# Optimization experiments

Measured on AMD Instinct MI355X. Metric: run time of the kernel, lower is better.

Reference implementation:

```python
import jax, jax.numpy as jnp
import numpy as np
import math

N_HEADS = 8
LN_EPS = 1e-5

def _layernorm(x, g, b):
    m = jnp.mean(x, axis=-1, keepdims=True)
    v = jnp.var(x, axis=-1, keepdims=True)
    return (x - m) / jnp.sqrt(v + LN_EPS) * g + b

def _elu_feature(x):
    return jax.nn.elu(x) + 1.0

def _recurrence(Q, K, V, decay, reverse):
    # Q,K,V: (B,H,T,d); decay: (H,)
    B, H, T, d = Q.shape
    lamS = decay[None, :, None, None]
    lamz = decay[None, :, None]
    def step(carry, inp):
        S, z = carry
        q, k, v = inp
        S = lamS * S + k[..., :, None] * v[..., None, :]       # (B,H,d,d)
        z = lamz * z + k                                        # (B,H,d)
        y_raw = jnp.einsum('bhd,bhde->bhe', q, S)
        c_raw = jnp.sum(q * z, axis=-1)
        qk = jnp.sum(q * k, axis=-1, keepdims=True)
        return (S, z), (y_raw - 0.5 * qk * v, c_raw - 0.5 * qk[..., 0])
    S0 = jnp.zeros((B, H, d, d), Q.dtype)
    z0 = jnp.zeros((B, H, d), Q.dtype)
    qs = jnp.moveaxis(Q, 2, 0)
    ks = jnp.moveaxis(K, 2, 0)
    vs = jnp.moveaxis(V, 2, 0)
    _, (Y, C) = jax.lax.scan(step, (S0, z0), (qs, ks, vs), reverse=reverse)
    return jnp.moveaxis(Y, 0, 2), jnp.moveaxis(C, 0, 2)  # (B,H,T,d),(B,H,T)

def setup_inputs() -> dict:
    B, T, D, F = 2, 2048, 512, 2048
    key = jax.random.key(0)
    ks = jax.random.split(key, 8)
    std = 0.02
    return {
        'x': jax.random.normal(ks[0], (B, T, D), jnp.float32),
        'mask': jnp.zeros((B, T), dtype=bool),
        'Wq': jax.random.normal(ks[1], (D, D), jnp.float32) * std,
        'Wk': jax.random.normal(ks[2], (D, D), jnp.float32) * std,
        'Wv': jax.random.normal(ks[3], (D, D), jnp.float32) * std,
        'Wo': jax.random.normal(ks[4], (D, D), jnp.float32) * std,
        'bo': jnp.zeros((D,), jnp.float32),
        'g1': jnp.ones((D,), jnp.float32),
        'b1': jnp.zeros((D,), jnp.float32),
        'g2': jnp.ones((D,), jnp.float32),
        'b2': jnp.zeros((D,), jnp.float32),
        'W1': jax.random.normal(ks[5], (F, D), jnp.float32) * std,
        'bf1': jnp.zeros((F,), jnp.float32),
        'W2': jax.random.normal(ks[6], (D, F), jnp.float32) * std,
        'bf2': jnp.zeros((D,), jnp.float32),
        'decay_logit': jnp.full((N_HEADS,), math.log(9.0), jnp.float32),
    }

def reference(x, mask, Wq, Wk, Wv, Wo, bo, g1, b1, g2, b2, W1, bf1, W2, bf2, decay_logit):
    B, T, D = x.shape
    H = N_HEADS
    hd = D // H
    residual = x
    xn = _layernorm(x, g1, b1)
    def proj(W):
        return jnp.einsum('btd,od->bto', xn, W).reshape(B, T, H, hd).transpose(0, 2, 1, 3)
    Q = _elu_feature(proj(Wq))
    K = _elu_feature(proj(Wk))
    V = proj(Wv)
    pad = (~mask).astype(x.dtype)[:, None, :, None]  # (B,1,T,1)
    K = K * pad
    V = V * pad
    decay = jax.nn.sigmoid(decay_logit)
    Yf, Cf = _recurrence(Q, K, V, decay, reverse=False)
    Yb, Cb = _recurrence(Q, K, V, decay, reverse=True)
    denom = jnp.clip((Cf + Cb)[..., None], 1e-6)
    out = (Yf + Yb) / denom                       # (B,H,T,d)
    out = out.transpose(0, 2, 1, 3).reshape(B, T, D)
    out = jnp.einsum('btd,od->bto', out, Wo) + bo
    x = residual + out
    h = _layernorm(x, g2, b2)
    ffn = jnp.einsum('btd,fd->btf', h, W1) + bf1
    ffn = jax.nn.gelu(ffn, approximate=False)
    ffn = jnp.einsum('btf,df->btd', ffn, W2) + bf2
    return x + ffn
```

## Files before the change

kernel.cpp:

```cpp
#include <hip/hip_runtime.h>
#include <math.h>

#define BB 2
#define TT 2048
#define DD 512
#define FF 2048
#define HH 8
#define BT 4096
#define NC 32
#define CK 64

typedef __bf16 bf16_t;
typedef bf16_t bf16x8 __attribute__((ext_vector_type(8)));
typedef bf16_t bf16x4 __attribute__((ext_vector_type(4)));
typedef float f32x4 __attribute__((ext_vector_type(4)));

typedef const __attribute__((address_space(1))) void* gas_p;
typedef __attribute__((address_space(3))) void* las_p;

__device__ __forceinline__ void async16(const void* g, void* l) {
  __builtin_amdgcn_global_load_lds((gas_p)g, (las_p)l, 16, 0, 0);
}

#define PIPE_SYNC(vm) asm volatile("s_waitcnt lgkmcnt(0) vmcnt(" vm ")\n\ts_barrier" ::: "memory")

__global__ __launch_bounds__(256) void ln_cast_kernel(
    const float* __restrict__ x, const float* __restrict__ g, const float* __restrict__ bb,
    bf16_t* __restrict__ out,
    const float* __restrict__ Wq, const float* __restrict__ Wk,
    const float* __restrict__ Wv, const float* __restrict__ Wo,
    const float* __restrict__ W1, const float* __restrict__ W2,
    bf16_t* __restrict__ wdst) {
  int t = threadIdx.x;
  if (blockIdx.x >= BT) {
    size_t i = ((size_t)(blockIdx.x - BT) * 256 + t) * 8;
    const float* src; size_t off;
    if (i < 262144)       { src = Wq; off = i; }
    else if (i < 524288)  { src = Wk; off = i - 262144; }
    else if (i < 786432)  { src = Wv; off = i - 524288; }
    else if (i < 1048576) { src = Wo; off = i - 786432; }
    else if (i < 2097152) { src = W1; off = i - 1048576; }
    else                  { src = W2; off = i - 2097152; }
    float4 a = *(const float4*)(src + off);
    float4 b = *(const float4*)(src + off + 4);
    bf16x8 o;
    o[0] = (bf16_t)a.x; o[1] = (bf16_t)a.y; o[2] = (bf16_t)a.z; o[3] = (bf16_t)a.w;
    o[4] = (bf16_t)b.x; o[5] = (bf16_t)b.y; o[6] = (bf16_t)b.z; o[7] = (bf16_t)b.w;
    *(bf16x8*)(wdst + i) = o;
    return;
  }
  int row = blockIdx.x;
  const float* xr = x + (size_t)row * DD;
  float v0 = xr[t], v1 = xr[t + 256];
  float s = v0 + v1, sq = v0 * v0 + v1 * v1;
  for (int o = 32; o; o >>= 1) { s += __shfl_down(s, o); sq += __shfl_down(sq, o); }
  __shared__ float red[8];
  __shared__ float mv[2];
  int w = t >> 6;
  if ((t & 63) == 0) { red[w] = s; red[4 + w] = sq; }
  __syncthreads();
  if (t == 0) {
    float S = red[0] + red[1] + red[2] + red[3];
    float Q = red[4] + red[5] + red[6] + red[7];
    float m = S * (1.f / 512.f);
    float var = Q * (1.f / 512.f) - m * m;
    mv[0] = m; mv[1] = rsqrtf(var + 1e-5f);
  }
  __syncthreads();
  float m = mv[0], r = mv[1];
  out[(size_t)row * DD + t]       = (bf16_t)((v0 - m) * r * g[t] + bb[t]);
  out[(size_t)row * DD + t + 256] = (bf16_t)((v1 - m) * r * g[t + 256] + bb[t + 256]);
}

template<int MODE>
__global__ __launch_bounds__(256) void mfma_gemm(
    const bf16_t* __restrict__ A, const bf16_t* __restrict__ B, int K, int NT,
    bf16_t* __restrict__ Qo, bf16_t* __restrict__ Ko, bf16_t* __restrict__ Vo,
    bf16_t* __restrict__ Ob, const float* __restrict__ bias,
    const unsigned char* __restrict__ mask) {
  __shared__ __align__(16) bf16_t smem[3 * 8192];
  int tid = threadIdx.x;
  int bid = blockIdx.x;
  int xcd = bid & 7;
  int tmp = bid >> 3;
  int nt = tmp % NT;
  int mt = (tmp / NT) * 8 + xcd;
  int n0 = nt * 128, m0 = mt * 128;
  int elt = tid * 8;
  int srow = elt >> 5, scol = elt & 31;
  const bf16_t* Ag = A + (size_t)(m0 + srow) * K + scol;
  const bf16_t* Bg = B + (size_t)(n0 + srow) * K + scol;
  size_t hstep = (size_t)64 * K;
  int NS = K >> 5;
#define ISSUE(s) { bf16_t* st = smem + ((s) % 3) * 8192; int k0 = (s) * 32; \
    async16(Ag + k0, st + elt); async16(Ag + k0 + hstep, st + 2048 + elt); \
    async16(Bg + k0, st + 4096 + elt); async16(Bg + k0 + hstep, st + 6144 + elt); }
  ISSUE(0); ISSUE(1);
  f32x4 acc[4][4] = {};
  int w = tid >> 6, l = tid & 63;
  int wm = (w >> 1) * 64, wn = (w & 1) * 64;
  int fr = l & 15, fk = (l >> 4) * 8;
  for (int i = 0; i < NS; i++) {
    if (i < NS - 1) PIPE_SYNC("4");
    else            PIPE_SYNC("0");
    if (i + 2 < NS) ISSUE(i + 2);
    const bf16_t* As = smem + (i % 3) * 8192;
    const bf16_t* Bs = As + 4096;
    bf16x8 af[4], bfr[4];
#pragma unroll
    for (int ii = 0; ii < 4; ii++) af[ii] = *(const bf16x8*)&As[(wm + ii * 16 + fr) * 32 + fk];
#pragma unroll
    for (int j = 0; j < 4; j++) bfr[j] = *(const bf16x8*)&Bs[(wn + j * 16 + fr) * 32 + fk];
#pragma unroll
    for (int ii = 0; ii < 4; ii++)
#pragma unroll
      for (int j = 0; j < 4; j++)
        acc[ii][j] = __builtin_amdgcn_mfma_f32_16x16x32_bf16(af[ii], bfr[j], acc[ii][j], 0, 0, 0);
  }
#undef ISSUE
  __syncthreads();
  const int CST = 136;
  int cn = l & 15, cr = (l >> 4) * 4;
  bf16_t* outp;
  int ldc, ncol0;
  if (MODE == 0) {
    int seg = n0 >> 9;
    outp = seg == 0 ? Qo : (seg == 1 ? Ko : Vo);
    ldc = 512; ncol0 = n0 & 511;
  } else {
    outp = Ob; ldc = 2048; ncol0 = n0;
  }
#pragma unroll
  for (int i = 0; i < 4; i++) {
#pragma unroll
    for (int r = 0; r < 4; r++) {
      int mrow = wm + i * 16 + cr + r;
      float p = 1.f;
      if (MODE == 0) p = mask[m0 + mrow] ? 0.f : 1.f;
#pragma unroll
      for (int j = 0; j < 4; j++) {
        int ncol = wn + j * 16 + cn;
        float v = acc[i][j][r];
        float ov;
        if (MODE == 0) {
          int seg = n0 >> 9;
          float e = v > 0.f ? v + 1.f : expf(v);
          ov = seg == 0 ? e : (seg == 1 ? e * p : v * p);
        } else {
          float t2 = v + bias[ncol0 + ncol];
          ov = 0.5f * t2 * (1.f + erff(t2 * 0.70710678118654752f));
        }
        smem[mrow * CST + ncol] = (bf16_t)ov;
      }
    }
  }
  __syncthreads();
#pragma unroll
  for (int it = 0; it < 8; it++) {
    int vec = tid + it * 256;
    int row = vec >> 4;
    int col = (vec & 15) * 8;
    bf16x8 v8 = *(const bf16x8*)&smem[row * CST + col];
    *(bf16x8*)(outp + (size_t)(m0 + row) * ldc + ncol0 + col) = v8;
  }
}

template<int KPER>
__global__ __launch_bounds__(256) void mfma_gemm_pk(
    const bf16_t* __restrict__ A, const bf16_t* __restrict__ B, int Kst,
    float* __restrict__ P0, float* __restrict__ P1) {
  __shared__ __align__(16) bf16_t smem[4 * 6144];
  int tid = threadIdx.x;
  int bid = blockIdx.x;
  int xcd = bid & 7;
  int tmp = bid >> 3;
  int nt = tmp & 7;
  int mt = (tmp >> 3) * 8 + xcd;
  int n0 = nt * 64, m0 = mt * 128;
  int kb = blockIdx.y * KPER;
  float* P = blockIdx.y ? P1 : P0;
  int elt = tid * 8;
  int arow = elt >> 5, acol = elt & 31;
  const bf16_t* Ag = A + (size_t)(m0 + arow) * Kst + acol;
  const bf16_t* Bg = B + (size_t)(n0 + arow) * Kst + acol;
  size_t hstep = (size_t)64 * Kst;
  const int NS = KPER >> 5;
#define ISSUE(s) { bf16_t* st = smem + ((s) & 3) * 6144; int k0 = kb + (s) * 32; \
    async16(Ag + k0, st + elt); async16(Ag + k0 + hstep, st + 2048 + elt); \
    async16(Bg + k0, st + 4096 + elt); }
  ISSUE(0); ISSUE(1); ISSUE(2);
  f32x4 acc[4][2] = {};
  int w = tid >> 6, l = tid & 63;
  int wm = (w >> 1) * 64, wn = (w & 1) * 32;
  int fr = l & 15, fk = (l >> 4) * 8;
  for (int i = 0; i < NS; i++) {
    int rem = NS - 1 - i;
    if (rem >= 2)      PIPE_SYNC("6");
    else if (rem == 1) PIPE_SYNC("3");
    else               PIPE_SYNC("0");
    if (i + 3 < NS) ISSUE(i + 3);
    const bf16_t* As = smem + (i & 3) * 6144;
    const bf16_t* Bs = As + 4096;
    bf16x8 af[4], bfr[2];
#pragma unroll
    for (int ii = 0; ii < 4; ii++) af[ii] = *(const bf16x8*)&As[(wm + ii * 16 + fr) * 32 + fk];
#pragma unroll
    for (int j = 0; j < 2; j++) bfr[j] = *(const bf16x8*)&Bs[(wn + j * 16 + fr) * 32 + fk];
#pragma unroll
    for (int ii = 0; ii < 4; ii++)
#pragma unroll
      for (int j = 0; j < 2; j++)
        acc[ii][j] = __builtin_amdgcn_mfma_f32_16x16x32_bf16(af[ii], bfr[j], acc[ii][j], 0, 0, 0);
  }
#undef ISSUE
  int cn = l & 15, cr = (l >> 4) * 4;
#pragma unroll
  for (int i = 0; i < 4; i++)
#pragma unroll
    for (int r = 0; r < 4; r++) {
      int m = m0 + wm + i * 16 + cr + r;
#pragma unroll
      for (int j = 0; j < 2; j++) {
        int n = n0 + wn + j * 16 + cn;
        P[(size_t)m * 512 + n] = acc[i][j][r];
      }
    }
}

__global__ __launch_bounds__(256) void reduce2_kernel(
    const float* __restrict__ P0, const float* __restrict__ P1,
    const float* __restrict__ bias, const float* __restrict__ resid,
    float* __restrict__ o) {
  size_t idx = ((size_t)blockIdx.x * 256 + threadIdx.x) * 4;
  int n = (int)(idx & 511);
  float4 a = *(const float4*)(P0 + idx);
  float4 b = *(const float4*)(P1 + idx);
  float4 rr = *(const float4*)(resid + idx);
  float4 bi = *(const float4*)(bias + n);
  *(float4*)(o + idx) = make_float4(a.x + b.x + bi.x + rr.x, a.y + b.y + bi.y + rr.y,
                                    a.z + b.z + bi.z + rr.z, a.w + b.w + bi.w + rr.w);
}

__global__ __launch_bounds__(256) void reduce_ln_kernel(
    const float* __restrict__ P0, const float* __restrict__ P1,
    const float* __restrict__ bias, const float* __restrict__ resid,
    float* __restrict__ x2, const float* __restrict__ g, const float* __restrict__ bb,
    bf16_t* __restrict__ out) {
  int row = blockIdx.x;
  int t = threadIdx.x;
  size_t o0 = (size_t)row * DD + t;
  size_t o1 = o0 + 256;
  float v0 = P0[o0] + P1[o0] + bias[t] + resid[o0];
  float v1 = P0[o1] + P1[o1] + bias[t + 256] + resid[o1];
  x2[o0] = v0; x2[o1] = v1;
  float s = v0 + v1, sq = v0 * v0 + v1 * v1;
  for (int o = 32; o; o >>= 1) { s += __shfl_down(s, o); sq += __shfl_down(sq, o); }
  __shared__ float red[8];
  __shared__ float mv[2];
  int w = t >> 6;
  if ((t & 63) == 0) { red[w] = s; red[4 + w] = sq; }
  __syncthreads();
  if (t == 0) {
    float S = red[0] + red[1] + red[2] + red[3];
    float Q = red[4] + red[5] + red[6] + red[7];
    float m = S * (1.f / 512.f);
    float var = Q * (1.f / 512.f) - m * m;
    mv[0] = m; mv[1] = rsqrtf(var + 1e-5f);
  }
  __syncthreads();
  float m = mv[0], r = mv[1];
  out[o0] = (bf16_t)((v0 - m) * r * g[t] + bb[t]);
  out[o1] = (bf16_t)((v1 - m) * r * g[t + 256] + bb[t + 256]);
}

__global__ __launch_bounds__(256) void chunk_summary_kernel(
    const bf16_t* __restrict__ Kb, const bf16_t* __restrict__ Vb,
    const float* __restrict__ dl, bf16_t* __restrict__ Sst, float* __restrict__ zst) {
  int chunk = blockIdx.x, bh = blockIdx.y;
  int b = bh >> 3, h = bh & 7;
  int t0 = chunk * CK;
  int tid = threadIdx.x;
  __shared__ __align__(16) float Ks[64][64];
  __shared__ __align__(16) float Vs[64][64];
  __shared__ float pw[72];
  float lam = 1.f / (1.f + expf(-dl[h]));
  if (tid <= 64) pw[tid] = powf(lam, (float)tid);
  int lrow = tid >> 2, lq = tid & 3;
  for (int q = 0; q < 2; q++) {
    int c = lq * 16 + q * 8;
    size_t g = ((size_t)(b * TT + t0 + lrow)) * DD + (size_t)h * 64 + c;
    bf16x8 k8 = *(const bf16x8*)(Kb + g);
    bf16x8 v8 = *(const bf16x8*)(Vb + g);
#pragma unroll
    for (int u = 0; u < 8; u++) { Ks[lrow][c + u] = (float)k8[u]; Vs[lrow][c + u] = (float)v8[u]; }
  }
  __syncthreads();
  int e1 = tid & 63;
  int e2b = (tid >> 6) * 16;
  float af_[16], ab_[16];
#pragma unroll
  for (int r = 0; r < 16; r++) { af_[r] = 0.f; ab_[r] = 0.f; }
  float zf = 0.f, zb = 0.f;
  for (int j = 0; j < 64; j++) {
    float kj = Ks[j][e1];
    float kf = pw[63 - j] * kj;
    float kb2 = pw[j] * kj;
    if (tid < 64) { zf += kf; zb += kb2; }
#pragma unroll
    for (int rr = 0; rr < 16; rr += 4) {
      float4 v4 = *(const float4*)&Vs[j][e2b + rr];
      af_[rr]     += kf * v4.x;  ab_[rr]     += kb2 * v4.x;
      af_[rr + 1] += kf * v4.y;  ab_[rr + 1] += kb2 * v4.y;
      af_[rr + 2] += kf * v4.z;  ab_[rr + 2] += kb2 * v4.z;
      af_[rr + 3] += kf * v4.w;  ab_[rr + 3] += kb2 * v4.w;
    }
  }
  size_t bf_ = (((size_t)bh * NC + chunk) * 64 + e1) * 64 + e2b;
  size_t bb_ = ((((size_t)16 + bh) * NC + chunk) * 64 + e1) * 64 + e2b;
  bf16x8 of0, of1, ob0, ob1;
#pragma unroll
  for (int u = 0; u < 8; u++) {
    of0[u] = (bf16_t)af_[u];     of1[u] = (bf16_t)af_[u + 8];
    ob0[u] = (bf16_t)ab_[u];     ob1[u] = (bf16_t)ab_[u + 8];
  }
  *(bf16x8*)(Sst + bf_) = of0;     *(bf16x8*)(Sst + bf_ + 8) = of1;
  *(bf16x8*)(Sst + bb_) = ob0;     *(bf16x8*)(Sst + bb_ + 8) = ob1;
  if (tid < 64) {
    zst[((size_t)bh * NC + chunk) * 64 + tid] = zf;
    zst[(((size_t)16 + bh) * NC + chunk) * 64 + tid] = zb;
  }
}

__global__ __launch_bounds__(1024) void scan_kernel(bf16_t* __restrict__ Sst,
                                                    float* __restrict__ zst,
                                                    const float* __restrict__ dl) {
  int bh = blockIdx.x, dir = blockIdx.y;
  int h = bh & 7;
  int tid = threadIdx.x;
  float lam = 1.f / (1.f + expf(-dl[h]));
  float lamC = powf(lam, 64.f);
  size_t base = ((size_t)dir * 16 + bh) * (size_t)NC * 4096 + (size_t)tid * 4;
  float s0 = 0.f, s1 = 0.f, s2 = 0.f, s3 = 0.f;
  for (int g = 0; g < 4; g++) {
    bf16x4 L[8];
#pragma unroll
    for (int i = 0; i < 8; i++) {
      int s = g * 8 + i;
      int c = dir ? (NC - 1 - s) : s;
      L[i] = *(bf16x4*)(Sst + base + (size_t)c * 4096);
    }
#pragma unroll
    for (int i = 0; i < 8; i++) {
      int s = g * 8 + i;
      int c = dir ? (NC - 1 - s) : s;
      s0 = s0 * lamC + (float)L[i][0];
      s1 = s1 * lamC + (float)L[i][1];
      s2 = s2 * lamC + (float)L[i][2];
      s3 = s3 * lamC + (float)L[i][3];
      bf16x4 o;
      o[0] = (bf16_t)s0; o[1] = (bf16_t)s1; o[2] = (bf16_t)s2; o[3] = (bf16_t)s3;
      *(bf16x4*)(Sst + base + (size_t)c * 4096) = o;
    }
  }
  if (tid < 64) {
    size_t zb = ((size_t)dir * 16 + bh) * (size_t)NC * 64 + tid;
    float z = 0.f;
    for (int g = 0; g < 4; g++) {
      float zL[8];
#pragma unroll
      for (int i = 0; i < 8; i++) {
        int s = g * 8 + i;
        int c = dir ? (NC - 1 - s) : s;
        zL[i] = zst[zb + (size_t)c * 64];
      }
#pragma unroll
      for (int i = 0; i < 8; i++) {
        int s = g * 8 + i;
        int c = dir ? (NC - 1 - s) : s;
        z = z * lamC + zL[i];
        zst[zb + (size_t)c * 64] = z;
      }
    }
  }
}

__global__ __launch_bounds__(256) void chunk_attn_kernel(
    const bf16_t* __restrict__ Qb, const bf16_t* __restrict__ Kb, const bf16_t* __restrict__ Vb,
    const bf16_t* __restrict__ Sst, const float* __restrict__ zst, const float* __restrict__ dl,
    bf16_t* __restrict__ attnb) {
  int chunk = blockIdx.x, bh = blockIdx.y;
  int b = bh >> 3, h = bh & 7;
  int t0 = chunk * CK;
  int tid = threadIdx.x;
  __shared__ __align__(16) float Qt[64][68];
  __shared__ __align__(16) float KtA[64][68];
  __shared__ __align__(16) float Vs[64][64];
  __shared__ __align__(16) bf16_t Spf[64][64];
  __shared__ __align__(16) bf16_t Spb[64][64];
  __shared__ float rowpart[64][16];
  __shared__ float zpf[64], zpb[64];
  __shared__ float den[64];
  __shared__ float pw[72];
  float lam = 1.f / (1.f + expf(-dl[h]));
  if (tid <= 64) pw[tid] = powf(lam, (float)tid);
  int lrow = tid >> 2, lq = tid & 3;
  for (int q = 0; q < 2; q++) {
    int c = lq * 16 + q * 8;
    size_t g = ((size_t)(b * TT + t0 + lrow)) * DD + (size_t)h * 64 + c;
    bf16x8 q8 = *(const bf16x8*)(Qb + g);
    bf16x8 k8 = *(const bf16x8*)(Kb + g);
    bf16x8 v8 = *(const bf16x8*)(Vb + g);
#pragma unroll
    for (int u = 0; u < 8; u++) {
      Qt[c + u][lrow] = (float)q8[u];
      KtA[c + u][lrow] = (float)k8[u];
      Vs[lrow][c + u] = (float)v8[u];
    }
  }
  {
    int c16 = lq * 16;
    if (chunk > 0) {
      const bf16_t* src = Sst + ((size_t)bh * NC + chunk - 1) * 4096 + (size_t)lrow * 64 + c16;
      *(bf16x8*)&Spf[lrow][c16] = *(const bf16x8*)src;
      *(bf16x8*)&Spf[lrow][c16 + 8] = *(const bf16x8*)(src + 8);
      if (tid < 64) zpf[tid] = zst[((size_t)bh * NC + chunk - 1) * 64 + tid];
    } else {
      bf16x8 z8 = {};
      *(bf16x8*)&Spf[lrow][c16] = z8;
      *(bf16x8*)&Spf[lrow][c16 + 8] = z8;
      if (tid < 64) zpf[tid] = 0.f;
    }
    if (chunk < NC - 1) {
      const bf16_t* src = Sst + (((size_t)16 + bh) * NC + chunk + 1) * 4096 + (size_t)lrow * 64 + c16;
      *(bf16x8*)&Spb[lrow][c16] = *(const bf16x8*)src;
      *(bf16x8*)&Spb[lrow][c16 + 8] = *(const bf16x8*)(src + 8);
      if (tid < 64) zpb[tid] = zst[(((size_t)16 + bh) * NC + chunk + 1) * 64 + tid];
    } else {
      bf16x8 z8 = {};
      *(bf16x8*)&Spb[lrow][c16] = z8;
      *(bf16x8*)&Spb[lrow][c16 + 8] = z8;
      if (tid < 64) zpb[tid] = 0.f;
    }
  }
  __syncthreads();
  int tx = tid & 15, ty = tid >> 4;
  int i0 = ty * 4, j0 = tx * 4;
  int e0 = tx * 4;
  float acc[4][4] = {};
  for (int d = 0; d < 64; d++) {
    float4 qf = *(const float4*)&Qt[d][i0];
    float4 kf = *(const float4*)&KtA[d][j0];
    float qa[4] = {qf.x, qf.y, qf.z, qf.w};
    float ka[4] = {kf.x, kf.y, kf.z, kf.w};
#pragma unroll
    for (int r = 0; r < 4; r++)
#pragma unroll
      for (int c = 0; c < 4; c++) acc[r][c] += qa[r] * ka[c];
  }
  __syncthreads();
  float rs[4] = {0.f, 0.f, 0.f, 0.f};
  float colv[4][4];
#pragma unroll
  for (int r = 0; r < 4; r++) {
    int i = i0 + r;
#pragma unroll
    for (int c = 0; c < 4; c++) {
      int j = j0 + c;
      int dd = i > j ? i - j : j - i;
      float v = acc[r][c] * pw[dd];
      rs[r] += v;
      colv[c][r] = v;
    }
  }
#pragma unroll
  for (int c = 0; c < 4; c++)
    *(float4*)&KtA[j0 + c][i0] = make_float4(colv[c][0], colv[c][1], colv[c][2], colv[c][3]);
#pragma unroll
  for (int r = 0; r < 4; r++) rowpart[i0 + r][tx] = rs[r];
  __syncthreads();
  float accY[4][4] = {}, accSf[4][4] = {}, accSb[4][4] = {};
  for (int j = 0; j < 64; j++) {
    float4 af = *(const float4*)&KtA[j][i0];
    float4 vf = *(const float4*)&Vs[j][e0];
    float aa[4] = {af.x, af.y, af.z, af.w};
    float vv[4] = {vf.x, vf.y, vf.z, vf.w};
#pragma unroll
    for (int r = 0; r < 4; r++)
#pragma unroll
      for (int c = 0; c < 4; c++) accY[r][c] += aa[r] * vv[c];
  }
  for (int d = 0; d < 64; d++) {
    float4 qf = *(const float4*)&Qt[d][i0];
    bf16x4 sf4 = *(const bf16x4*)&Spf[d][e0];
    bf16x4 sb4 = *(const bf16x4*)&Spb[d][e0];
    float qq[4] = {qf.x, qf.y, qf.z, qf.w};
    float sf[4] = {(float)sf4[0], (float)sf4[1], (float)sf4[2], (float)sf4[3]};
    float sb[4] = {(float)sb4[0], (float)sb4[1], (float)sb4[2], (float)sb4[3]};
#pragma unroll
    for (int r = 0; r < 4; r++)
#pragma unroll
      for (int c = 0; c < 4; c++) {
        accSf[r][c] += qq[r] * sf[c];
        accSb[r][c] += qq[r] * sb[c];
      }
  }
  if (tid < 64) {
    int i = tid;
    float s = 0.f;
#pragma unroll
    for (int xx = 0; xx < 16; xx++) s += rowpart[i][xx];
    float czf = 0.f, czb = 0.f;
    for (int d = 0; d < 64; d++) { czf += Qt[d][i] * zpf[d]; czb += Qt[d][i] * zpb[d]; }
    den[i] = s + pw[i + 1] * czf + pw[64 - i] * czb;
  }
  __syncthreads();
#pragma unroll
  for (int r = 0; r < 4; r++) {
    int i = i0 + r;
    float lrf = pw[i + 1], lrb = pw[64 - i];
    float inv = 1.f / fmaxf(den[i], 1e-6f);
    bf16x4 o;
#pragma unroll
    for (int c = 0; c < 4; c++)
      o[c] = (bf16_t)((accY[r][c] + lrf * accSf[r][c] + lrb * accSb[r][c]) * inv);
    *(bf16x4*)(attnb + ((size_t)(b * TT + t0 + i)) * DD + (size_t)h * 64 + e0) = o;
  }
}

extern "C" void kernel_launch(void* const* d_in, const int* in_sizes, int n_in,
                              void* d_out, int out_size, void* d_ws, size_t ws_size,
                              hipStream_t stream) {
  const float* x   = (const float*)d_in[0];
  const unsigned char* mask = (const unsigned char*)d_in[1];
  const float* Wq  = (const float*)d_in[2];
  const float* Wk  = (const float*)d_in[3];
  const float* Wv  = (const float*)d_in[4];
  const float* Wo  = (const float*)d_in[5];
  const float* bo  = (const float*)d_in[6];
  const float* g1  = (const float*)d_in[7];
  const float* b1  = (const float*)d_in[8];
  const float* g2  = (const float*)d_in[9];
  const float* b2  = (const float*)d_in[10];
  const float* W1  = (const float*)d_in[11];
  const float* bf1 = (const float*)d_in[12];
  const float* W2  = (const float*)d_in[13];
  const float* bf2 = (const float*)d_in[14];
  const float* dl  = (const float*)d_in[15];
  float* out = (float*)d_out;

  float* ws = (float*)d_ws;
  const size_t U = (size_t)BT * DD;
  float* Qr  = ws;
  float* Kr  = ws + U;
  float* Vr  = ws + 2 * U;
  float* R3  = ws + 3 * U;
  float* R4  = ws + 4 * U;
  float* x2  = ws + 5 * U;
  bf16_t* Sstb = (bf16_t*)(ws + 6 * U);
  float* zst = ws + 8 * U;
  bf16_t* wall = (bf16_t*)(ws + 8 * U + 131072);
  bf16_t* Qb    = (bf16_t*)Qr;
  bf16_t* Kb    = (bf16_t*)Kr;
  bf16_t* Vb    = (bf16_t*)Vr;
  bf16_t* xnb   = (bf16_t*)R3;
  bf16_t* attnb = (bf16_t*)x2;
  bf16_t* h2b   = (bf16_t*)Qr;
  bf16_t* ffn1b = (bf16_t*)Kr;
  bf16_t* Wob = wall + 786432;
  bf16_t* W1b = wall + 1048576;
  bf16_t* W2b = wall + 2097152;
  float* Ps0 = R3;
  float* Ps1 = R4;

  ln_cast_kernel<<<BT + 1536, 256, 0, stream>>>(x, g1, b1, xnb, Wq, Wk, Wv, Wo, W1, W2, wall);
  mfma_gemm<0><<<384, 256, 0, stream>>>(xnb, wall, 512, 12, Qb, Kb, Vb,
                                        nullptr, nullptr, mask);
  chunk_summary_kernel<<<dim3(NC, 16), 256, 0, stream>>>(Kb, Vb, dl, Sstb, zst);
  scan_kernel<<<dim3(16, 2), 1024, 0, stream>>>(Sstb, zst, dl);
  chunk_attn_kernel<<<dim3(NC, 16), 256, 0, stream>>>(Qb, Kb, Vb, Sstb, zst, dl, attnb);
  mfma_gemm_pk<256><<<dim3(256, 2), 256, 0, stream>>>(attnb, Wob, 512, Ps0, Ps1);
  reduce_ln_kernel<<<BT, 256, 0, stream>>>(Ps0, Ps1, bo, x, x2, g2, b2, h2b);
  mfma_gemm<2><<<512, 256, 0, stream>>>(h2b, W1b, 512, 16, nullptr, nullptr, nullptr,
                                        ffn1b, bf1, nullptr);
  mfma_gemm_pk<1024><<<dim3(256, 2), 256, 0, stream>>>(ffn1b, W2b, 2048, Ps0, Ps1);
  reduce2_kernel<<<2048, 256, 0, stream>>>(Ps0, Ps1, bf2, x2, out);
}
```

Before: 216.6 us.

## Use bf16 MFMA for intra-chunk attention and store chunk states transposed

Replaces the fp32 scalar FMA tiles in chunk_attn_kernel with bf16 16x16x32 MFMA for the QK^T, AV and Q·S products, keeping operands in bf16 padded shared arrays. The chunk-state kernel now writes S transposed so the MFMA B-operand can be loaded row-contiguously. The aim is to cut ALU time in the attention chunk kernel. In exchange, the decayed score matrix is rounded to bf16 before the AV product, which lowers precision, and the state and output stores become scalar and strided rather than vectorised.

Measured after the change: 207.8 us. 1.04x faster.

```diff
diff --git a/kernel.cpp b/kernel.cpp
--- a/kernel.cpp
+++ b/kernel.cpp
@@ -315,16 +315,13 @@
       af_[rr + 3] += kf * v4.w;  ab_[rr + 3] += kb2 * v4.w;
     }
   }
-  size_t bf_ = (((size_t)bh * NC + chunk) * 64 + e1) * 64 + e2b;
-  size_t bb_ = ((((size_t)16 + bh) * NC + chunk) * 64 + e1) * 64 + e2b;
-  bf16x8 of0, of1, ob0, ob1;
-#pragma unroll
-  for (int u = 0; u < 8; u++) {
-    of0[u] = (bf16_t)af_[u];     of1[u] = (bf16_t)af_[u + 8];
-    ob0[u] = (bf16_t)ab_[u];     ob1[u] = (bf16_t)ab_[u + 8];
-  }
-  *(bf16x8*)(Sst + bf_) = of0;     *(bf16x8*)(Sst + bf_ + 8) = of1;
-  *(bf16x8*)(Sst + bb_) = ob0;     *(bf16x8*)(Sst + bb_ + 8) = ob1;
+  size_t bfr = ((size_t)bh * NC + chunk) * 4096;
+  size_t bbr = (((size_t)16 + bh) * NC + chunk) * 4096;
+#pragma unroll
+  for (int r = 0; r < 16; r++) {
+    Sst[bfr + (size_t)(e2b + r) * 64 + e1] = (bf16_t)af_[r];
+    Sst[bbr + (size_t)(e2b + r) * 64 + e1] = (bf16_t)ab_[r];
+  }
   if (tid < 64) {
     zst[((size_t)bh * NC + chunk) * 64 + tid] = zf;
     zst[(((size_t)16 + bh) * NC + chunk) * 64 + tid] = zb;
@@ -384,6 +381,7 @@
   }
 }
 
+#define AST 72
 __global__ __launch_bounds__(256) void chunk_attn_kernel(
     const bf16_t* __restrict__ Qb, const bf16_t* __restrict__ Kb, const bf16_t* __restrict__ Vb,
     const bf16_t* __restrict__ Sst, const float* __restrict__ zst, const float* __restrict__ dl,
@@ -392,11 +390,11 @@
   int b = bh >> 3, h = bh & 7;
   int t0 = chunk * CK;
   int tid = threadIdx.x;
-  __shared__ __align__(16) float Qt[64][68];
-  __shared__ __align__(16) float KtA[64][68];
-  __shared__ __align__(16) float Vs[64][64];
-  __shared__ __align__(16) bf16_t Spf[64][64];
-  __shared__ __align__(16) bf16_t Spb[64][64];
+  __shared__ __align__(16) bf16_t Qa[64 * AST];
+  __shared__ __align__(16) bf16_t KA[64 * AST];
+  __shared__ __align__(16) bf16_t Vt[64 * AST];
+  __shared__ __align__(16) bf16_t Sft[64 * AST];
+  __shared__ __align__(16) bf16_t Sbt[64 * AST];
   __shared__ float rowpart[64][16];
   __shared__ float zpf[64], zpb[64];
   __shared__ float den[64];
@@ -410,99 +408,85 @@
     bf16x8 q8 = *(const bf16x8*)(Qb + g);
     bf16x8 k8 = *(const bf16x8*)(Kb + g);
     bf16x8 v8 = *(const bf16x8*)(Vb + g);
-#pragma unroll
-    for (int u = 0; u < 8; u++) {
-      Qt[c + u][lrow] = (float)q8[u];
-      KtA[c + u][lrow] = (float)k8[u];
-      Vs[lrow][c + u] = (float)v8[u];
-    }
+    *(bf16x8*)&Qa[lrow * AST + c] = q8;
+    *(bf16x8*)&KA[lrow * AST + c] = k8;
+#pragma unroll
+    for (int u = 0; u < 8; u++) Vt[(c + u) * AST + lrow] = v8[u];
   }
   {
     int c16 = lq * 16;
     if (chunk > 0) {
       const bf16_t* src = Sst + ((size_t)bh * NC + chunk - 1) * 4096 + (size_t)lrow * 64 + c16;
-      *(bf16x8*)&Spf[lrow][c16] = *(const bf16x8*)src;
-      *(bf16x8*)&Spf[lrow][c16 + 8] = *(const bf16x8*)(src + 8);
+      *(bf16x8*)&Sft[lrow * AST + c16] = *(const bf16x8*)src;
+      *(bf16x8*)&Sft[lrow * AST + c16 + 8] = *(const bf16x8*)(src + 8);
       if (tid < 64) zpf[tid] = zst[((size_t)bh * NC + chunk - 1) * 64 + tid];
     } else {
       bf16x8 z8 = {};
-      *(bf16x8*)&Spf[lrow][c16] = z8;
-      *(bf16x8*)&Spf[lrow][c16 + 8] = z8;
+      *(bf16x8*)&Sft[lrow * AST + c16] = z8;
+      *(bf16x8*)&Sft[lrow * AST + c16 + 8] = z8;
       if (tid < 64) zpf[tid] = 0.f;
     }
     if (chunk < NC - 1) {
       const bf16_t* src = Sst + (((size_t)16 + bh) * NC + chunk + 1) * 4096 + (size_t)lrow * 64 + c16;
-      *(bf16x8*)&Spb[lrow][c16] = *(const bf16x8*)src;
-      *(bf16x8*)&Spb[lrow][c16 + 8] = *(const bf16x8*)(src + 8);
+      *(bf16x8*)&Sbt[lrow * AST + c16] = *(const bf16x8*)src;
+      *(bf16x8*)&Sbt[lrow * AST + c16 + 8] = *(const bf16x8*)(src + 8);
       if (tid < 64) zpb[tid] = zst[(((size_t)16 + bh) * NC + chunk + 1) * 64 + tid];
     } else {
       bf16x8 z8 = {};
-      *(bf16x8*)&Spb[lrow][c16] = z8;
-      *(bf16x8*)&Spb[lrow][c16 + 8] = z8;
+      *(bf16x8*)&Sbt[lrow * AST + c16] = z8;
+      *(bf16x8*)&Sbt[lrow * AST + c16 + 8] = z8;
       if (tid < 64) zpb[tid] = 0.f;
     }
   }
   __syncthreads();
-  int tx = tid & 15, ty = tid >> 4;
-  int i0 = ty * 4, j0 = tx * 4;
-  int e0 = tx * 4;
-  float acc[4][4] = {};
-  for (int d = 0; d < 64; d++) {
-    float4 qf = *(const float4*)&Qt[d][i0];
-    float4 kf = *(const float4*)&KtA[d][j0];
-    float qa[4] = {qf.x, qf.y, qf.z, qf.w};
-    float ka[4] = {kf.x, kf.y, kf.z, kf.w};
-#pragma unroll
-    for (int r = 0; r < 4; r++)
-#pragma unroll
-      for (int c = 0; c < 4; c++) acc[r][c] += qa[r] * ka[c];
+  int w = tid >> 6, l = tid & 63;
+  int fr = l & 15, fk = (l >> 4) * 8;
+  int cr = (l >> 4) * 4, cn = l & 15;
+  int ms = w * 16;
+  bf16x8 qf0 = *(const bf16x8*)&Qa[(ms + fr) * AST + fk];
+  bf16x8 qf1 = *(const bf16x8*)&Qa[(ms + fr) * AST + 32 + fk];
+  f32x4 aqk[4] = {};
+#pragma unroll
+  for (int t = 0; t < 4; t++) {
+    bf16x8 kf0 = *(const bf16x8*)&KA[(t * 16 + fr) * AST + fk];
+    bf16x8 kf1 = *(const bf16x8*)&KA[(t * 16 + fr) * AST + 32 + fk];
+    aqk[t] = __builtin_amdgcn_mfma_f32_16x16x32_bf16(qf0, kf0, aqk[t], 0, 0, 0);
+    aqk[t] = __builtin_amdgcn_mfma_f32_16x16x32_bf16(qf1, kf1, aqk[t], 0, 0, 0);
   }
   __syncthreads();
   float rs[4] = {0.f, 0.f, 0.f, 0.f};
-  float colv[4][4];
-#pragma unroll
-  for (int r = 0; r < 4; r++) {
-    int i = i0 + r;
-#pragma unroll
-    for (int c = 0; c < 4; c++) {
-      int j = j0 + c;
+#pragma unroll
+  for (int t = 0; t < 4; t++) {
+#pragma unroll
+    for (int r = 0; r < 4; r++) {
+      int i = ms + cr + r;
+      int j = t * 16 + cn;
       int dd = i > j ? i - j : j - i;
-      float v = acc[r][c] * pw[dd];
+      float v = aqk[t][r] * pw[dd];
       rs[r] += v;
-      colv[c][r] = v;
-    }
-  }
-#pragma unroll
-  for (int c = 0; c < 4; c++)
-    *(float4*)&KtA[j0 + c][i0] = make_float4(colv[c][0], colv[c][1], colv[c][2], colv[c][3]);
-#pragma unroll
-  for (int r = 0; r < 4; r++) rowpart[i0 + r][tx] = rs[r];
-  __syncthreads();
-  float accY[4][4] = {}, accSf[4][4] = {}, accSb[4][4] = {};
-  for (int j = 0; j < 64; j++) {
-    float4 af = *(const float4*)&KtA[j][i0];
-    float4 vf = *(const float4*)&Vs[j][e0];
-    float aa[4] = {af.x, af.y, af.z, af.w};
-    float vv[4] = {vf.x, vf.y, vf.z, vf.w};
-#pragma unroll
-    for (int r = 0; r < 4; r++)
-#pragma unroll
-      for (int c = 0; c < 4; c++) accY[r][c] += aa[r] * vv[c];
-  }
-  for (int d = 0; d < 64; d++) {
-    float4 qf = *(const float4*)&Qt[d][i0];
-    bf16x4 sf4 = *(const bf16x4*)&Spf[d][e0];
-    bf16x4 sb4 = *(const bf16x4*)&Spb[d][e0];
-    float qq[4] = {qf.x, qf.y, qf.z, qf.w};
-    float sf[4] = {(float)sf4[0], (float)sf4[1], (float)sf4[2], (float)sf4[3]};
-    float sb[4] = {(float)sb4[0], (float)sb4[1], (float)sb4[2], (float)sb4[3]};
-#pragma unroll
-    for (int r = 0; r < 4; r++)
-#pragma unroll
-      for (int c = 0; c < 4; c++) {
-        accSf[r][c] += qq[r] * sf[c];
-        accSb[r][c] += qq[r] * sb[c];
-      }
+      KA[i * AST + j] = (bf16_t)v;
+    }
+  }
+#pragma unroll
+  for (int r = 0; r < 4; r++) rowpart[ms + cr + r][cn] = rs[r];
+  __syncthreads();
+  bf16x8 af0 = *(const bf16x8*)&KA[(ms + fr) * AST + fk];
+  bf16x8 af1 = *(const bf16x8*)&KA[(ms + fr) * AST + 32 + fk];
+  f32x4 aY[4] = {}, aSf[4] = {}, aSb[4] = {};
+#pragma unroll
+  for (int t = 0; t < 4; t++) {
+    bf16x8 vf0 = *(const bf16x8*)&Vt[(t * 16 + fr) * AST + fk];
+    bf16x8 vf1 = *(const bf16x8*)&Vt[(t * 16 + fr) * AST + 32 + fk];
+    aY[t] = __builtin_amdgcn_mfma_f32_16x16x32_bf16(af0, vf0, aY[t], 0, 0, 0);
+    aY[t] = __builtin_amdgcn_mfma_f32_16x16x32_bf16(af1, vf1, aY[t], 0, 0, 0);
+    bf16x8 sf0 = *(const bf16x8*)&Sft[(t * 16 + fr) * AST + fk];
+    bf16x8 sf1 = *(const bf16x8*)&Sft[(t * 16 + fr) * AST + 32 + fk];
+    aSf[t] = __builtin_amdgcn_mfma_f32_16x16x32_bf16(qf0, sf0, aSf[t], 0, 0, 0);
+    aSf[t] = __builtin_amdgcn_mfma_f32_16x16x32_bf16(qf1, sf1, aSf[t], 0, 0, 0);
+    bf16x8 sb0 = *(const bf16x8*)&Sbt[(t * 16 + fr) * AST + fk];
+    bf16x8 sb1 = *(const bf16x8*)&Sbt[(t * 16 + fr) * AST + 32 + fk];
+    aSb[t] = __builtin_amdgcn_mfma_f32_16x16x32_bf16(qf0, sb0, aSb[t], 0, 0, 0);
+    aSb[t] = __builtin_amdgcn_mfma_f32_16x16x32_bf16(qf1, sb1, aSb[t], 0, 0, 0);
   }
   if (tid < 64) {
     int i = tid;
@@ -510,20 +494,25 @@
 #pragma unroll
     for (int xx = 0; xx < 16; xx++) s += rowpart[i][xx];
     float czf = 0.f, czb = 0.f;
-    for (int d = 0; d < 64; d++) { czf += Qt[d][i] * zpf[d]; czb += Qt[d][i] * zpb[d]; }
+    for (int c = 0; c < 64; c += 8) {
+      bf16x8 q8 = *(const bf16x8*)&Qa[i * AST + c];
+#pragma unroll
+      for (int u = 0; u < 8; u++) { czf += (float)q8[u] * zpf[c + u]; czb += (float)q8[u] * zpb[c + u]; }
+    }
     den[i] = s + pw[i + 1] * czf + pw[64 - i] * czb;
   }
   __syncthreads();
 #pragma unroll
-  for (int r = 0; r < 4; r++) {
-    int i = i0 + r;
-    float lrf = pw[i + 1], lrb = pw[64 - i];
-    float inv = 1.f / fmaxf(den[i], 1e-6f);
-    bf16x4 o;
-#pragma unroll
-    for (int c = 0; c < 4; c++)
-      o[c] = (bf16_t)((accY[r][c] + lrf * accSf[r][c] + lrb * accSb[r][c]) * inv);
-    *(bf16x4*)(attnb + ((size_t)(b * TT + t0 + i)) * DD + (size_t)h * 64 + e0) = o;
+  for (int t = 0; t < 4; t++) {
+#pragma unroll
+    for (int r = 0; r < 4; r++) {
+      int i = ms + cr + r;
+      int e = t * 16 + cn;
+      float lrf = pw[i + 1], lrb = pw[64 - i];
+      float inv = 1.f / fmaxf(den[i], 1e-6f);
+      float val = (aY[t][r] + lrf * aSf[t][r] + lrb * aSb[t][r]) * inv;
+      attnb[((size_t)(b * TT + t0 + i)) * DD + (size_t)h * 64 + e] = (bf16_t)val;
+    }
   }
 }
 
```
